# Kernel tuning notes

Measured on AMD Instinct MI355X. Metric: run time of the kernel, lower is better.

Reference implementation:

```python
import jax, jax.numpy as jnp
import numpy as np

DISPS = (8, 8, 4, 2)
STRIDES = (2, 1, 1, 1)
DG = 4      # deformable groups
PAD = 1     # (kernel_size-1)//2 for k=3
KH = KW = 3


def pointwise_corr(f1, f2, disp, stride):
    """Windowed pointwise cross-correlation.
    f1, f2: [B, C, H, W]. Returns [B, (2d+1)^2, H, W], dy-major shift order,
    displacement step = stride, normalized by channel count.
    """
    B, C, H, W = f1.shape
    pad = disp * stride
    f2p = jnp.pad(f2, ((0, 0), (0, 0), (pad, pad), (pad, pad)))
    rng = np.arange(2 * disp + 1) * stride
    shifts = np.stack(np.meshgrid(rng, rng, indexing='ij'), -1).reshape(-1, 2)
    shifts = jnp.asarray(shifts, jnp.int32)

    def one(s):
        f2s = jax.lax.dynamic_slice(f2p, (0, 0, s[0], s[1]), (B, C, H, W))
        return jnp.sum(f1 * f2s, axis=1) / C   # [B, H, W]

    corr = jax.vmap(one)(shifts)               # [K2, B, H, W]
    return jnp.transpose(corr, (1, 0, 2, 3))


def bilinear_sample(img, y, x):
    """img: [cg, H, W]; y, x: [K2, H, W] float sample coords.
    Zero outside boundaries (deform-conv semantics). Returns [cg, K2, H, W]."""
    cg, H, W = img.shape
    y0 = jnp.floor(y); x0 = jnp.floor(x)
    wy = y - y0;       wx = x - x0
    y0i = y0.astype(jnp.int32); x0i = x0.astype(jnp.int32)

    def gather(iy, ix):
        valid = (iy >= 0) & (iy < H) & (ix >= 0) & (ix < W)
        v = img[:, jnp.clip(iy, 0, H - 1), jnp.clip(ix, 0, W - 1)]  # [cg,K2,H,W]
        return v * valid.astype(img.dtype)

    v00 = gather(y0i,     x0i)
    v01 = gather(y0i,     x0i + 1)
    v10 = gather(y0i + 1, x0i)
    v11 = gather(y0i + 1, x0i + 1)
    return (v00 * (1 - wy) * (1 - wx) + v01 * (1 - wy) * wx
            + v10 * wy * (1 - wx) + v11 * wy * wx)


def deform_conv(x, offset, weight, dg, pad):
    """Deformable conv v1, stride 1. x: [N,C,H,W]; offset: [N, dg*2*K2, H, W]
    (per group, per kernel point, (dy,dx)); weight: [O, C, kh, kw]."""
    N, C, H, W = x.shape
    O, _, kh, kw = weight.shape
    K2 = kh * kw
    cg = C // dg
    off = offset.reshape(N, dg, K2, 2, H, W)
    ky, kx = np.meshgrid(np.arange(kh), np.arange(kw), indexing='ij')
    ky = jnp.asarray(ky.reshape(-1), jnp.float32)
    kx = jnp.asarray(kx.reshape(-1), jnp.float32)
    gy = jnp.arange(H, dtype=jnp.float32)
    gx = jnp.arange(W, dtype=jnp.float32)
    base_y = ky[:, None, None] - pad + gy[None, :, None]   # [K2,H,1]
    base_x = kx[:, None, None] - pad + gx[None, None, :]   # [K2,1,W]
    ys = base_y[None, None] + off[:, :, :, 0]              # [N,dg,K2,H,W]
    xs = base_x[None, None] + off[:, :, :, 1]
    xg = x.reshape(N, dg, cg, H, W)
    sampled = jax.vmap(jax.vmap(bilinear_sample))(xg, ys, xs)  # [N,dg,cg,K2,H,W]
    w = weight.reshape(O, dg, cg, K2)
    return jnp.einsum('ogck,ngckhw->nohw', w, sampled)


def _forward_single(x, w_off, w_adapt, disp, stride):
    T, B, C, H, W = x.shape
    corrs = [pointwise_corr(x[t], x[t - 1], disp, stride) for t in range(1, T)]
    corr = jnp.concatenate(corrs, axis=0)                   # [(T-1)*B, K2, H, W]
    offset = jnp.einsum('ok,bkhw->bohw', w_off, corr)       # 1x1 conv, no bias
    feat_in = x[1:].reshape((T - 1) * B, C, H, W)
    feat = jax.nn.relu(deform_conv(feat_in, offset, w_adapt, DG, PAD))
    return jnp.concatenate([x[0], feat], axis=0)            # [T*B, C, H, W]


def setup_inputs() -> dict:
    key = jax.random.key(0)
    ks = jax.random.split(key, 12)
    shapes = [(2, 2, 256, 64, 64), (2, 2, 256, 32, 32),
              (2, 2, 256, 16, 16), (2, 2, 256, 8, 8)]
    d = {}
    for i, s in enumerate(shapes):
        d[f"x{i}"] = jax.random.normal(ks[i], s, jnp.float32)
    for i, disp in enumerate(DISPS):
        K2 = (2 * disp + 1) ** 2
        d[f"w_off{i}"] = 0.01 * jax.random.normal(ks[4 + i], (DG * 2 * KH * KW, K2), jnp.float32)
        d[f"w_adapt{i}"] = 0.01 * jax.random.normal(ks[8 + i], (256, 256, KH, KW), jnp.float32)
    return d


def reference(x0, x1, x2, x3, w_off0, w_off1, w_off2, w_off3,
              w_adapt0, w_adapt1, w_adapt2, w_adapt3):
    xs = [x0, x1, x2, x3]
    w_offs = [w_off0, w_off1, w_off2, w_off3]
    w_adapts = [w_adapt0, w_adapt1, w_adapt2, w_adapt3]
    outs = [_forward_single(xs[l], w_offs[l], w_adapts[l], DISPS[l], STRIDES[l])
            for l in range(4)]
    return tuple(outs)
```

## Files before the change

### kernel.cpp

```cpp
#include <hip/hip_runtime.h>

typedef unsigned int u32;
typedef unsigned short u16;
typedef _Float16 f16x2 __attribute__((ext_vector_type(2)));
typedef _Float16 f16x8 __attribute__((ext_vector_type(8)));
typedef __bf16 bf16x8 __attribute__((ext_vector_type(8)));
typedef float f32x4 __attribute__((ext_vector_type(4)));

static __device__ __forceinline__ f16x2 bch(u32 u) { return __builtin_bit_cast(f16x2, u); }


__global__ __launch_bounds__(256) void prep_kernel(
    const float* __restrict__ x0, const float* __restrict__ x1,
    const float* __restrict__ x2, const float* __restrict__ x3,
    const float* __restrict__ w0, const float* __restrict__ w1,
    const float* __restrict__ w2, const float* __restrict__ w3,
    u32* __restrict__ xq, u16* __restrict__ A, float* __restrict__ offs,
    float* __restrict__ out)
{
  __shared__ u32 plds[32 * 65];
  int bx = blockIdx.x, t = threadIdx.x;
  if (bx < 3060) {
    int i = bx * 256 + t;
    if (i < 783360) offs[i] = 0.f;
    return;
  }
  if (bx < 4420) {
    int local = bx - 3060;
    const float* xs; int lvlb, lgW, lgnch;
    if (local < 1024)      { xs = x0; lvlb = 0;       lgW = 6; lgnch = 6; }
    else if (local < 1280) { xs = x1; lvlb = 2097152; lgW = 5; lgnch = 4; local -= 1024; }
    else if (local < 1344) { xs = x2; lvlb = 2621440; lgW = 4; lgnch = 2; local -= 1280; }
    else                   { xs = x3; lvlb = 2752512; lgW = 3; lgnch = 0; local -= 1344; }
    int HW = 1 << (2 * lgW);
    int hc = local & ((1 << lgnch) - 1);
    int g  = (local >> lgnch) & 3;
    int tb = local >> (lgnch + 2);
    int hw0 = hc * 64;
    int lane = t & 63, qd = t >> 6;
#pragma unroll
    for (int j = 0; j < 8; ++j) {
      int cpw = qd * 8 + j;
      int c = tb * 256 + g * 64 + cpw * 2;
      const float* s = xs + (size_t)c * HW + hw0 + lane;
      float f0 = s[0], f1 = s[HW];
      f16x2 h; h[0] = (_Float16)f0; h[1] = (_Float16)f1;
      plds[cpw * 65 + lane] = __builtin_bit_cast(u32, h);
    }
    __syncthreads();
    u32* dst = xq + lvlb + (size_t)(tb * 4 + g) * HW * 32 + (size_t)hw0 * 32;
#pragma unroll
    for (int j = 0; j < 8; ++j) {
      int ow = j * 256 + t;
      int hwl = ow >> 5, ww = ow & 31;
      dst[(size_t)hwl * 32 + ww] = plds[ww * 65 + hwl];
    }
    return;
  }
  if (bx < 8516) {
    int u = bx - 4420;
    int lv = u >> 10;
    int rest = u & 1023;
    int o = rest >> 2, g = rest & 3;
    const float* w = (lv == 0) ? w0 : (lv == 1) ? w1 : (lv == 2) ? w2 : w3;
    const float* src = w + (size_t)(o * 256 + g * 64) * 9;
    float* fl = (float*)plds;
    if (t < 256) { fl[t] = src[t]; fl[t + 256] = src[t + 256]; }
    if (t < 64)  { fl[t + 512] = src[t + 512]; }
    __syncthreads();
    u16* dst = A + (size_t)lv * 589824 + (size_t)o * 2304 + g * 576;
    if (t < 256) {
#pragma unroll
      for (int j = 0; j < 2; ++j) {
        int i = t + j * 256;
        int c = i & 63, p = i >> 6;
        __bf16 bv = (__bf16)fl[c * 9 + p];
        dst[i] = __builtin_bit_cast(u16, bv);
      }
    }
    if (t < 64) {
      int i = t + 512;
      int c = i & 63, p = i >> 6;
      __bf16 bv = (__bf16)fl[c * 9 + p];
      dst[i] = __builtin_bit_cast(u16, bv);
    }
    return;
  }
  {
    int i = (bx - 8516) * 256 + t;
    const float* xs; int base4, dst4;
    if (i < 524288)      { xs = x0; base4 = 0;      dst4 = 0; }
    else if (i < 655360) { xs = x1; base4 = 524288; dst4 = 1048576; }
    else if (i < 688128) { xs = x2; base4 = 655360; dst4 = 1310720; }
    else if (i < 696320) { xs = x3; base4 = 688128; dst4 = 1376256; }
    else return;
    int local = i - base4;
    ((float4*)out)[(size_t)dst4 + local] = ((const float4*)xs)[local];
  }
}

__global__ __launch_bounds__(256) void corr_mfma_kernel(const u32* __restrict__ xq, float* __restrict__ corr)
{
  __shared__ __align__(16) u32 lds[8192];
  int t = threadIdx.x, bx = blockIdx.x;

  if (bx >= 1472) {
    int gw = ((bx - 1472) * 256 + t) >> 6;
    int lane = t & 63;
    int cs = lane >> 4, hwi = lane & 15;
    int obase = gw * 16;
    int K2, R, DISP, lgW, xqlb, crb, rel;
    if (obase < 41472)      { K2 = 81; R = 9; DISP = 4; lgW = 4; xqlb = 2621440; crb = 2959360; rel = obase; }
    else if (obase < 44672) { K2 = 25; R = 5; DISP = 2; lgW = 3; xqlb = 2752512; crb = 3000832; rel = obase - 41472; }
    else return;
    int W = 1 << lgW, HW = W * W;
    int hw = (rel & (HW - 1)) + hwi;
    int rr = rel >> (2 * lgW);
    int k = rr % K2, b = rr / K2;
    int h = hw >> lgW, wc = hw & (W - 1);
    int dy = k / R - DISP, dx = k % R - DISP;
    int h2 = h + dy, w2 = wc + dx;
    float a = 0.f;
    if ((u32)h2 < (u32)W && (u32)w2 < (u32)W) {
      const u32* q1 = xq + xqlb + ((size_t)((2 + b) * 4 + cs) * HW + hw) * 32;
      const u32* q0 = xq + xqlb + ((size_t)(b * 4 + cs) * HW + (h2 * W + w2)) * 32;
#pragma unroll 8
      for (int j = 0; j < 32; ++j)
        a = __builtin_amdgcn_fdot2(bch(q1[j]), bch(q0[j]), a, false);
    }
    a += __shfl_xor(a, 16);
    a += __shfl_xor(a, 32);
    if (cs == 0) corr[crb + rel + hwi] = a * 0.00390625f;
    return;
  }

  int sbx = (bx & 7) * 184 + (bx >> 3);
  int l = t & 63, w = t >> 6;
  int lvl, b, y, kq, lgW, W, HW, xqlb, crb;
  if (sbx < 1152) { lvl = 0; int r = sbx;        kq = r % 9; r /= 9; y = r & 63; b = r >> 6;
                    lgW = 6; W = 64; HW = 4096; xqlb = 0;       crb = 0; }
  else            { lvl = 1; int r = sbx - 1152; kq = r % 5; r /= 5; y = r & 31; b = r >> 5;
                    lgW = 5; W = 32; HW = 1024; xqlb = 2097152; crb = 2367488; }
  int par, qy, storeok;
  if (lvl == 0) { int rr = w >> 1; par = w & 1; qy = (kq < 8) ? 2 * kq + rr : 16;
                  storeok = !(kq == 8 && w >= 2); }
  else          { par = 0; qy = 4 * kq + w; storeok = (qy <= 16); if (qy > 16) qy = 16; }
  int rowY = (lvl == 0) ? (y + 2 * qy - 16) : (y + qy - 8);
  int f1words = (lvl == 0) ? 1024 : 512;
  int tb1 = 2 + b, tb0 = b;

  bool f1do = (lvl == 0) || (w < 2);
  u32 f1_lo; int f1_dw;
  {
    int G = w * 64 + l;
    int px = G >> 2, s = G & 3;
    int i = px & 31;
    int pari = px >> 5;
    int x = (lvl == 0) ? (2 * i + pari) : px;
    int cg = (s ^ ((i & 3) ^ ((i >> 2) & 3))) & 3;
    f1_lo = (u32)(xqlb + (y * W + x) * 32 + cg * 4);
    f1_dw = w * 256;
  }
  u32 f2_lo[3], f2_mask[3]; int f2_dw[3];
#pragma unroll
  for (int q = 0; q < 3; ++q) {
    int F = q * 64 + l;
    int jp = F >> 2, s = F & 3;
    int cg = (s ^ ((jp & 3) ^ ((jp >> 2) & 3))) & 3;
    int xs = (lvl == 0) ? (2 * (jp - 8) + par) : (jp - 8);
    bool valid = ((u32)xs < (u32)W) && ((u32)rowY < (u32)W);
    f2_lo[q]   = valid ? (u32)(xqlb + (rowY * W + xs) * 32 + cg * 4) : 6968960u;
    f2_mask[q] = valid ? 0xFFFFFFFFu : 0u;
    f2_dw[q]   = f1words + w * 768 + q * 256;
  }
  int lr = l & 15, lk = l >> 4;
  int aoff[2], boff[3];
#pragma unroll
  for (int it = 0; it < 2; ++it) {
    int iA = it * 16 + lr;
    int px = ((lvl == 0) ? par * 32 : 0) + iA;
    int phys = (lk ^ ((iA & 3) ^ ((iA >> 2) & 3))) & 3;
    aoff[it] = (px * 16 + phys * 4) * 4;
  }
#pragma unroll
  for (int T = 0; T < 3; ++T) {
    int jp = T * 16 + lr;
    int phys = (lk ^ ((jp & 3) ^ ((jp >> 2) & 3))) & 3;
    boff[T] = (f1words + w * 768 + jp * 16 + phys * 4) * 4;
  }

  f32x4 acc0 = {0,0,0,0}, acc1 = {0,0,0,0}, acc2 = {0,0,0,0}, acc3 = {0,0,0,0};

  auto issue = [&](int ch, int sel) {
    int g2 = ch >> 1, hf = ch & 1;
    u32 cb1 = ((u32)(tb1 * 4 + g2) * (u32)HW) * 32u + (u32)hf * 16u;
    u32 cb0 = ((u32)(tb0 * 4 + g2) * (u32)HW) * 32u + (u32)hf * 16u;
    u32* lb = &lds[sel * 4096];
    if (f1do)
      __builtin_amdgcn_global_load_lds(xq + cb1 + f1_lo, lb + f1_dw, 16, 0, 0);
#pragma unroll
    for (int q = 0; q < 3; ++q)
      __builtin_amdgcn_global_load_lds(xq + ((cb0 & f2_mask[q]) + f2_lo[q]), lb + f2_dw[q], 16, 0, 0);
  };

  issue(0, 0);
#pragma unroll 1
  for (int ch = 0; ch < 8; ++ch) {
    int sel = ch & 1;
    asm volatile("s_waitcnt vmcnt(0)" ::: "memory");
    asm volatile("s_barrier" ::: "memory");
    __builtin_amdgcn_sched_barrier(0);
    if (ch < 7) issue(ch + 1, sel ^ 1);
    const char* lb = (const char*)&lds[sel * 4096];
    f16x8 A0 = *(const f16x8*)(lb + aoff[0]);
    f16x8 A1 = *(const f16x8*)(lb + aoff[1]);
    f16x8 B0 = *(const f16x8*)(lb + boff[0]);
    f16x8 B1 = *(const f16x8*)(lb + boff[1]);
    f16x8 B2 = *(const f16x8*)(lb + boff[2]);
    acc0 = __builtin_amdgcn_mfma_f32_16x16x32_f16(A0, B0, acc0, 0, 0, 0);
    acc1 = __builtin_amdgcn_mfma_f32_16x16x32_f16(A0, B1, acc1, 0, 0, 0);
    acc2 = __builtin_amdgcn_mfma_f32_16x16x32_f16(A1, B1, acc2, 0, 0, 0);
    acc3 = __builtin_amdgcn_mfma_f32_16x16x32_f16(A1, B2, acc3, 0, 0, 0);
  }

  if (!storeok) return;
  const float sc = 0.00390625f;
#pragma unroll
  for (int tile = 0; tile < 4; ++tile) {
    int it = (tile >= 2) ? 1 : 0;
    int T  = (tile == 0) ? 0 : (tile == 3) ? 2 : 1;
    f32x4 av = (tile == 0) ? acc0 : (tile == 1) ? acc1 : (tile == 2) ? acc2 : acc3;
    int jp = T * 16 + lr;
#pragma unroll
    for (int jj = 0; jj < 4; ++jj) {
      int i = it * 16 + lk * 4 + jj;
      int qx = jp - i;
      if (qx >= 0 && qx <= 16) {
        int xo = (lvl == 0) ? (2 * i + par) : i;
        int k = qy * 17 + qx;
        corr[crb + (size_t)(b * 289 + k) * HW + y * W + xo] = av[jj] * sc;
      }
    }
  }
}

__global__ __launch_bounds__(256) void offset_kernel(
    const float* __restrict__ corr,
    const float* __restrict__ wo0, const float* __restrict__ wo1,
    const float* __restrict__ wo2, const float* __restrict__ wo3,
    float* __restrict__ offs, float* __restrict__ part, int mode)
{
  int t = threadIdx.x, bx = blockIdx.x;
  int kc = bx % 6;
  int unit = bx / 6;
  int og = unit & 3;
  int pb = unit >> 2;

  int lgW, K2, crb, ofb, pbl;
  const float* wo;
  if (pb < 32)      { pbl = pb;      lgW = 6; K2 = 289; crb = 0;       ofb = 0;      wo = wo0; }
  else if (pb < 40) { pbl = pb - 32; lgW = 5; K2 = 289; crb = 2367488; ofb = 589824; wo = wo1; }
  else if (pb < 42) { pbl = pb - 40; lgW = 4; K2 = 81;  crb = 2959360; ofb = 737280; wo = wo2; }
  else              { pbl = 0;       lgW = 3; K2 = 25;  crb = 3000832; ofb = 774144; wo = wo3; }
  int HW = 1 << (2 * lgW);
  int pxg = pbl * 256 + t;
  if (lgW == 3 && t >= 128) return;
  int b = pxg >> (2 * lgW);
  int hw = pxg & (HW - 1);

  int kchunk = (K2 + 5) / 6;
  int klo = kc * kchunk;
  int khi = klo + kchunk; if (khi > K2) khi = K2;
  if (klo >= khi && mode == 0) return;
  if (khi < klo) khi = klo;

  const float* cr = corr + crb + (size_t)b * K2 * HW + hw;
  const float* wp = wo + (size_t)og * 18 * K2;
  float acc[18];
#pragma unroll
  for (int j = 0; j < 18; ++j) acc[j] = 0.f;
#pragma unroll 2
  for (int k = klo; k < khi; ++k) {
    float cv = cr[(size_t)k * HW];
#pragma unroll
    for (int j = 0; j < 18; ++j) acc[j] = fmaf(wp[(size_t)j * K2 + k], cv, acc[j]);
  }
  size_t lin = (size_t)ofb + ((size_t)b * 72 + og * 18) * HW + hw;
  if (mode) {
    float* op = part + (size_t)kc * 783360 + lin;
#pragma unroll
    for (int j = 0; j < 18; ++j) op[(size_t)j * HW] = acc[j];
  } else {
    float* op = offs + lin;
#pragma unroll
    for (int j = 0; j < 18; ++j) atomicAdd(&op[(size_t)j * HW], acc[j]);
  }
}

__global__ __launch_bounds__(256) void reduce_kernel(const float* __restrict__ part, float* __restrict__ offs)
{
  int i = blockIdx.x * 256 + threadIdx.x;
  if (i >= 195840) return;
  float4 s = ((const float4*)part)[i];
#pragma unroll
  for (int kc = 1; kc < 6; ++kc) {
    float4 v = ((const float4*)(part + (size_t)kc * 783360))[i];
    s.x += v.x; s.y += v.y; s.z += v.z; s.w += v.w;
  }
  ((float4*)offs)[i] = s;
}

__global__ __launch_bounds__(256) void sample_kernel(
    const u32* __restrict__ xq, const float* __restrict__ offs,
    u16* __restrict__ Bbuf, int Rg0, int nrows)
{
  int bx = blockIdx.x, nbk = gridDim.x;
  int bxs = ((nbk & 7) == 0) ? ((bx & 7) * (nbk >> 3) + (bx >> 3)) : bx;
  int tid = bxs * 256 + threadIdx.x;
  if (tid >= nrows * 144) return;
  int r_l = tid / 144;
  int rem = tid - r_l * 144;
  int gp = rem >> 2, cq = rem & 3;
  int Rg = Rg0 + r_l;
  int b, hw, lgW, xqlb, ofb;
  if (Rg < 8192)       { b = Rg >> 12;       hw = Rg & 4095;  lgW = 6; xqlb = 0;       ofb = 0; }
  else if (Rg < 10240) { int r = Rg - 8192;  b = r >> 10; hw = r & 1023; lgW = 5; xqlb = 2097152; ofb = 589824; }
  else if (Rg < 10752) { int r = Rg - 10240; b = r >> 8;  hw = r & 255;  lgW = 4; xqlb = 2621440; ofb = 737280; }
  else                 { int r = Rg - 10752; b = r >> 6;  hw = r & 63;   lgW = 3; xqlb = 2752512; ofb = 774144; }
  int W = 1 << lgW, HW = W * W;
  u16* rowp = Bbuf + (size_t)r_l * 2304;

  size_t ob = (size_t)ofb + ((size_t)b * 72 + gp * 2) * HW + hw;
  float ody = offs[ob], odx = offs[ob + HW];
  int g = gp / 9, p = gp - g * 9;
  int ky = p / 3, kx = p - ky * 3;
  int sh = hw >> lgW, sw = hw & (W - 1);
  float ys = (float)(sh + ky - 1) + ody;
  float xs = (float)(sw + kx - 1) + odx;
  float y0f = floorf(ys), x0f = floorf(xs);
  float wy = ys - y0f, wx = xs - x0f;
  int y0 = (int)y0f, x0 = (int)x0f, y1 = y0 + 1, x1 = x0 + 1;
  bool vy0 = (u32)y0 < (u32)W, vy1 = (u32)y1 < (u32)W;
  bool vx0 = (u32)x0 < (u32)W, vx1 = (u32)x1 < (u32)W;
  float w00 = (1.f - wy) * (1.f - wx), w01 = (1.f - wy) * wx;
  float w10 = wy * (1.f - wx), w11 = wy * wx;
  const u32* base = xq + xqlb + ((size_t)((2 + b) * 4 + g) * HW) * 32 + cq * 8;
  const uint4 z = make_uint4(0, 0, 0, 0);
  uint4 a00 = z, c00 = z, a01 = z, c01 = z, a10 = z, c10 = z, a11 = z, c11 = z;
  if (vy0 && vx0) { const u32* p0 = base + (size_t)(y0 * W + x0) * 32; a00 = *(const uint4*)p0; c00 = *(const uint4*)(p0 + 4); }
  if (vy0 && vx1) { const u32* p0 = base + (size_t)(y0 * W + x1) * 32; a01 = *(const uint4*)p0; c01 = *(const uint4*)(p0 + 4); }
  if (vy1 && vx0) { const u32* p0 = base + (size_t)(y1 * W + x0) * 32; a10 = *(const uint4*)p0; c10 = *(const uint4*)(p0 + 4); }
  if (vy1 && vx1) { const u32* p0 = base + (size_t)(y1 * W + x1) * 32; a11 = *(const uint4*)p0; c11 = *(const uint4*)(p0 + 4); }
  bf16x8 r0, r1;
#pragma unroll
  for (int ww = 0; ww < 4; ++ww) {
    f16x2 h00 = bch(((const u32*)&a00)[ww]);
    f16x2 h01 = bch(((const u32*)&a01)[ww]);
    f16x2 h10 = bch(((const u32*)&a10)[ww]);
    f16x2 h11 = bch(((const u32*)&a11)[ww]);
    float lo = w00 * (float)h00[0] + w01 * (float)h01[0] + w10 * (float)h10[0] + w11 * (float)h11[0];
    float hi = w00 * (float)h00[1] + w01 * (float)h01[1] + w10 * (float)h10[1] + w11 * (float)h11[1];
    r0[2 * ww] = (__bf16)lo; r0[2 * ww + 1] = (__bf16)hi;
  }
#pragma unroll
  for (int ww = 0; ww < 4; ++ww) {
    f16x2 h00 = bch(((const u32*)&c00)[ww]);
    f16x2 h01 = bch(((const u32*)&c01)[ww]);
    f16x2 h10 = bch(((const u32*)&c10)[ww]);
    f16x2 h11 = bch(((const u32*)&c11)[ww]);
    float lo = w00 * (float)h00[0] + w01 * (float)h01[0] + w10 * (float)h10[0] + w11 * (float)h11[0];
    float hi = w00 * (float)h00[1] + w01 * (float)h01[1] + w10 * (float)h10[1] + w11 * (float)h11[1];
    r1[2 * ww] = (__bf16)lo; r1[2 * ww + 1] = (__bf16)hi;
  }
  u16* dst = rowp + gp * 64 + cq * 16;
  *(bf16x8*)dst = r0;
  *(bf16x8*)(dst + 8) = r1;
}

#define G_ISSUE(P, kt) { const uint4* as_ = (const uint4*)(Asrc + (kt) * 64); \
                         const uint4* bs_ = (const uint4*)(Bsrc + (kt) * 64); \
                         a0##P = as_[0]; a1##P = as_[1]; b0##P = bs_[0]; b1##P = bs_[1]; }
#define G_COMMIT(P, sel) { *(uint4*)(&Al[sel][srow * 72 + sc4 * 16]) = a0##P; \
                           *(uint4*)(&Al[sel][srow * 72 + sc4 * 16 + 8]) = a1##P; \
                           *(uint4*)(&Bl[sel][srow * 72 + sc4 * 16]) = b0##P; \
                           *(uint4*)(&Bl[sel][srow * 72 + sc4 * 16 + 8]) = b1##P; }
#define G_MFMA(sel) { _Pragma("unroll") \
  for (int kk = 0; kk < 2; ++kk) { \
    bf16x8 fb0 = *(const bf16x8*)(&Bl[sel][(wvc * 32 + lr) * 72 + kk * 32 + lk * 8]); \
    bf16x8 fb1 = *(const bf16x8*)(&Bl[sel][(wvc * 32 + 16 + lr) * 72 + kk * 32 + lk * 8]); \
    bf16x8 fa0 = *(const bf16x8*)(&Al[sel][(wvr * 32 + lr) * 72 + kk * 32 + lk * 8]); \
    bf16x8 fa1 = *(const bf16x8*)(&Al[sel][(wvr * 32 + 16 + lr) * 72 + kk * 32 + lk * 8]); \
    acc[0][0] = __builtin_amdgcn_mfma_f32_16x16x32_bf16(fa0, fb0, acc[0][0], 0, 0, 0); \
    acc[0][1] = __builtin_amdgcn_mfma_f32_16x16x32_bf16(fa0, fb1, acc[0][1], 0, 0, 0); \
    acc[1][0] = __builtin_amdgcn_mfma_f32_16x16x32_bf16(fa1, fb0, acc[1][0], 0, 0, 0); \
    acc[1][1] = __builtin_amdgcn_mfma_f32_16x16x32_bf16(fa1, fb1, acc[1][1], 0, 0, 0); \
  } }

__global__ __launch_bounds__(256) void gemm2_kernel(
    const u16* __restrict__ A, const u16* __restrict__ Bbuf,
    int Rg0, float* __restrict__ out)
{
  __shared__ __align__(16) u16 Al[2][64 * 72];
  __shared__ __align__(16) u16 Bl[2][64 * 72];
  int t = threadIdx.x, bx = blockIdx.x;
  int nb = gridDim.x;
  int gsw = (bx & 7) * (nb >> 3) + (bx >> 3);
  int mt = gsw & 3, nt = gsw >> 2;
  int Rgt = Rg0 + nt * 64;
  int b, hw0, lgW, Ab, outb;
  if (Rgt < 8192)       { b = Rgt >> 12;       hw0 = Rgt & 4095;  lgW = 6; Ab = 0;       outb = 2097152; }
  else if (Rgt < 10240) { int r = Rgt - 8192;  b = r >> 10; hw0 = r & 1023; lgW = 5; Ab = 589824;  outb = 4718592; }
  else if (Rgt < 10752) { int r = Rgt - 10240; b = r >> 8;  hw0 = r & 255;  lgW = 4; Ab = 1179648; outb = 5373952; }
  else                  { int r = Rgt - 10752; b = r >> 6;  hw0 = r & 63;   lgW = 3; Ab = 1769472; outb = 5537792; }
  int HW = 1 << (2 * lgW);
  const u16* Bbase = Bbuf + (size_t)(Rgt - Rg0) * 2304;

  int o0 = mt * 64;
  int l = t & 63, wv = t >> 6;
  int lr = l & 15, lk = l >> 4;
  int wvr = wv >> 1, wvc = wv & 1;

  int srow = t >> 2, sc4 = t & 3;
  const u16* Asrc = A + Ab + (size_t)(o0 + srow) * 2304 + sc4 * 16;
  const u16* Bsrc = Bbase + (size_t)srow * 2304 + sc4 * 16;

  f32x4 acc[2][2];
#pragma unroll
  for (int i = 0; i < 2; ++i)
#pragma unroll
    for (int j = 0; j < 2; ++j) acc[i][j] = (f32x4){0, 0, 0, 0};

  uint4 a0A, a1A, b0A, b1A, a0B, a1B, b0B, b1B;

  G_ISSUE(A, 0); G_COMMIT(A, 0);
  G_ISSUE(B, 1);
  G_ISSUE(A, 2);
  __syncthreads();
#pragma unroll 1
  for (int k2 = 0; k2 < 18; ++k2) {
    int kt = 2 * k2;
    G_MFMA(0);
    if (kt < 35) G_COMMIT(B, 1);
    __syncthreads();
    if (kt + 3 < 36) G_ISSUE(B, kt + 3);
    G_MFMA(1);
    if (kt + 1 < 35) G_COMMIT(A, 0);
    __syncthreads();
    if (kt + 4 < 36) G_ISSUE(A, kt + 4);
  }

  float* op = out + outb + (size_t)b * 256 * HW;
#pragma unroll
  for (int ar = 0; ar < 2; ++ar)
#pragma unroll
    for (int bc = 0; bc < 2; ++bc)
#pragma unroll
      for (int j = 0; j < 4; ++j) {
        int orow = o0 + wvr * 32 + ar * 16 + lk * 4 + j;
        int col = hw0 + wvc * 32 + bc * 16 + lr;
        op[(size_t)orow * HW + col] = fmaxf(acc[ar][bc][j], 0.f);
      }
}

extern "C" void kernel_launch(void* const* d_in, const int* in_sizes, int n_in,
                              void* d_out, int out_size, void* d_ws, size_t ws_size,
                              hipStream_t stream) {
  const float* x[4];
  const float* woff[4];
  const float* wad[4];
  for (int l = 0; l < 4; ++l) {
    x[l]    = (const float*)d_in[l];
    woff[l] = (const float*)d_in[4 + 2 * l];
    wad[l]  = (const float*)d_in[5 + 2 * l];
  }
  float* out = (float*)d_out;
  char* ws = (char*)d_ws;
  u32*   xq   = (u32*)(ws);
  u16*   A    = (u16*)(ws + 11141120);
  float* corr = (float*)(ws + 15859712);
  float* offs = (float*)(ws + 27875840);
  float* part = (float*)(ws + 31009280);
  u16* BbufS = (u16*)(ws + 15859712);
  u16* BbufL = (u16*)(ws + 31009280);
  int big  = (ws_size >= (size_t)81144320) ? 1 : 0;
  int part_ok = (ws_size >= (size_t)(31009280 + 18800640)) ? 1 : 0;

  prep_kernel<<<11236, 256, 0, stream>>>(x[0], x[1], x[2], x[3],
                                         wad[0], wad[1], wad[2], wad[3], xq, A, offs, out);
  corr_mfma_kernel<<<2170, 256, 0, stream>>>(xq, corr);
  offset_kernel<<<1032, 256, 0, stream>>>(corr, woff[0], woff[1], woff[2], woff[3],
                                          offs, part, part_ok);
  if (part_ok)
    reduce_kernel<<<765, 256, 0, stream>>>(part, offs);

  if (big) {
    sample_kernel<<<6120, 256, 0, stream>>>(xq, offs, BbufL, 0, 10880);
    gemm2_kernel<<<680, 256, 0, stream>>>(A, BbufL, 0, out);
  } else {
    for (int ph = 0; ph < 5; ++ph) {
      int Rg0 = ph * 2560;
      int nrows = (ph < 4) ? 2560 : 640;
      int sgrid = (nrows * 144 + 255) / 256;
      int ggrid = (nrows / 64) * 4;
      sample_kernel<<<sgrid, 256, 0, stream>>>(xq, offs, BbufS, Rg0, nrows);
      gemm2_kernel<<<ggrid, 256, 0, stream>>>(A, BbufS, Rg0, out);
    }
  }
}
```

Measured before the change: 116.3 us.

## Triple-buffer corr LDS loads and remap offset kernel warps to output groups

The correlation MFMA kernel now triple-buffers its LDS tiles and keeps two chunks of global->LDS loads in flight. It waits with a partial vmcnt instead of draining all loads each iteration. To make the vmcnt count uniform, every wave now issues the f1 load, using a masked dummy address when it has no f1 work. Separately, the offset kernel now assigns the four offset groups to the four waves of a block over 64 shared pixels, which reuses corr reads within a block and trims the grid. The cost is more LDS per block, which may lower occupancy, plus some redundant dummy loads.

```diff
diff --git a/kernel.cpp b/kernel.cpp
--- a/kernel.cpp
+++ b/kernel.cpp
@@ -101,7 +101,7 @@
 
 __global__ __launch_bounds__(256) void corr_mfma_kernel(const u32* __restrict__ xq, float* __restrict__ corr)
 {
-  __shared__ __align__(16) u32 lds[8192];
+  __shared__ __align__(16) u32 lds[12288];
   int t = threadIdx.x, bx = blockIdx.x;
 
   if (bx >= 1472) {
@@ -150,7 +150,7 @@
   int tb1 = 2 + b, tb0 = b;
 
   bool f1do = (lvl == 0) || (w < 2);
-  u32 f1_lo; int f1_dw;
+  u32 f1_lo, f1_mask; int f1_dw;
   {
     int G = w * 64 + l;
     int px = G >> 2, s = G & 3;
@@ -158,8 +158,15 @@
     int pari = px >> 5;
     int x = (lvl == 0) ? (2 * i + pari) : px;
     int cg = (s ^ ((i & 3) ^ ((i >> 2) & 3))) & 3;
-    f1_lo = (u32)(xqlb + (y * W + x) * 32 + cg * 4);
-    f1_dw = w * 256;
+    if (f1do) {
+      f1_lo = (u32)(xqlb + (y * W + x) * 32 + cg * 4);
+      f1_dw = w * 256;
+      f1_mask = 0xFFFFFFFFu;
+    } else {
+      f1_lo = 6968960u;
+      f1_dw = 3584 + (w - 2) * 256;
+      f1_mask = 0u;
+    }
   }
   u32 f2_lo[3], f2_mask[3]; int f2_dw[3];
 #pragma unroll
@@ -196,22 +203,22 @@
     u32 cb1 = ((u32)(tb1 * 4 + g2) * (u32)HW) * 32u + (u32)hf * 16u;
     u32 cb0 = ((u32)(tb0 * 4 + g2) * (u32)HW) * 32u + (u32)hf * 16u;
     u32* lb = &lds[sel * 4096];
-    if (f1do)
-      __builtin_amdgcn_global_load_lds(xq + cb1 + f1_lo, lb + f1_dw, 16, 0, 0);
+    __builtin_amdgcn_global_load_lds(xq + ((cb1 & f1_mask) + f1_lo), lb + f1_dw, 16, 0, 0);
 #pragma unroll
     for (int q = 0; q < 3; ++q)
       __builtin_amdgcn_global_load_lds(xq + ((cb0 & f2_mask[q]) + f2_lo[q]), lb + f2_dw[q], 16, 0, 0);
   };
 
   issue(0, 0);
+  issue(1, 1);
 #pragma unroll 1
   for (int ch = 0; ch < 8; ++ch) {
-    int sel = ch & 1;
-    asm volatile("s_waitcnt vmcnt(0)" ::: "memory");
+    if (ch < 7) asm volatile("s_waitcnt vmcnt(4)" ::: "memory");
+    else        asm volatile("s_waitcnt vmcnt(0)" ::: "memory");
     asm volatile("s_barrier" ::: "memory");
     __builtin_amdgcn_sched_barrier(0);
-    if (ch < 7) issue(ch + 1, sel ^ 1);
-    const char* lb = (const char*)&lds[sel * 4096];
+    if (ch + 2 < 8) issue(ch + 2, (ch + 2) % 3);
+    const char* lb = (const char*)&lds[(ch % 3) * 4096];
     f16x8 A0 = *(const f16x8*)(lb + aoff[0]);
     f16x8 A1 = *(const f16x8*)(lb + aoff[1]);
     f16x8 B0 = *(const f16x8*)(lb + boff[0]);
@@ -253,20 +260,17 @@
   int t = threadIdx.x, bx = blockIdx.x;
   int kc = bx % 6;
   int unit = bx / 6;
-  int og = unit & 3;
-  int pb = unit >> 2;
-
-  int lgW, K2, crb, ofb, pbl;
+  int og = t >> 6;
+  int lane = t & 63;
+  int pxg = unit * 64 + lane;
+
+  int b, hw, lgW, K2, crb, ofb;
   const float* wo;
-  if (pb < 32)      { pbl = pb;      lgW = 6; K2 = 289; crb = 0;       ofb = 0;      wo = wo0; }
-  else if (pb < 40) { pbl = pb - 32; lgW = 5; K2 = 289; crb = 2367488; ofb = 589824; wo = wo1; }
-  else if (pb < 42) { pbl = pb - 40; lgW = 4; K2 = 81;  crb = 2959360; ofb = 737280; wo = wo2; }
-  else              { pbl = 0;       lgW = 3; K2 = 25;  crb = 3000832; ofb = 774144; wo = wo3; }
+  if (pxg < 8192)       { b = pxg >> 12;        hw = pxg & 4095; lgW = 6; K2 = 289; crb = 0;       ofb = 0;      wo = wo0; }
+  else if (pxg < 10240) { int r = pxg - 8192;  b = r >> 10; hw = r & 1023; lgW = 5; K2 = 289; crb = 2367488; ofb = 589824; wo = wo1; }
+  else if (pxg < 10752) { int r = pxg - 10240; b = r >> 8;  hw = r & 255;  lgW = 4; K2 = 81;  crb = 2959360; ofb = 737280; wo = wo2; }
+  else                  { int r = pxg - 10752; b = r >> 6;  hw = r & 63;   lgW = 3; K2 = 25;  crb = 3000832; ofb = 774144; wo = wo3; }
   int HW = 1 << (2 * lgW);
-  int pxg = pbl * 256 + t;
-  if (lgW == 3 && t >= 128) return;
-  int b = pxg >> (2 * lgW);
-  int hw = pxg & (HW - 1);
 
   int kchunk = (K2 + 5) / 6;
   int klo = kc * kchunk;
@@ -488,7 +492,7 @@
   prep_kernel<<<11236, 256, 0, stream>>>(x[0], x[1], x[2], x[3],
                                          wad[0], wad[1], wad[2], wad[3], xq, A, offs, out);
   corr_mfma_kernel<<<2170, 256, 0, stream>>>(xq, corr);
-  offset_kernel<<<1032, 256, 0, stream>>>(corr, woff[0], woff[1], woff[2], woff[3],
+  offset_kernel<<<1020, 256, 0, stream>>>(corr, woff[0], woff[1], woff[2], woff[3],
                                           offs, part, part_ok);
   if (part_ok)
     reduce_kernel<<<765, 256, 0, stream>>>(part, offs);
```

New measurement: 153.7 us. 1.32x slower.
